# Optimization experiments

Measured on AMD Instinct MI355X. Metric: run time of the kernel, lower is better.

The kernel has to match this reference:

```python
import jax, jax.numpy as jnp
import numpy as np
import math

N_HEAD = 16

def setup_inputs() -> dict:
    key = jax.random.key(0)
    ks = jax.random.split(key, 5)
    B, T, C = 4, 2048, 1024
    x = jax.random.normal(ks[0], (B, T, C), dtype=jnp.float32)
    # xavier-uniform-ish scale for dense kernels
    W_attn = jax.random.normal(ks[1], (C, 3 * C), dtype=jnp.float32) * (1.0 / math.sqrt(C))
    b_attn = jnp.zeros((3 * C,), dtype=jnp.float32)
    W_proj = jax.random.normal(ks[2], (C, C), dtype=jnp.float32) * (1.0 / math.sqrt(C))
    b_proj = jnp.zeros((C,), dtype=jnp.float32)
    return {"x": x, "W_attn": W_attn, "b_attn": b_attn, "W_proj": W_proj, "b_proj": b_proj}

def reference(x, W_attn, b_attn, W_proj, b_proj):
    B, T, C = x.shape
    H = N_HEAD
    D = C // H
    qkv = x @ W_attn + b_attn                      # [B,T,3C]
    q, k, v = jnp.split(qkv, 3, axis=-1)
    q = q.reshape(B, T, H, D).transpose(0, 2, 1, 3)  # [B,H,T,D]
    k = k.reshape(B, T, H, D).transpose(0, 2, 1, 3)
    v = v.reshape(B, T, H, D).transpose(0, 2, 1, 3)
    att = jnp.einsum("bhqd,bhkd->bhqk", q, k) * (1.0 / math.sqrt(D))  # [B,H,T,T]
    causal = jnp.tril(jnp.ones((T, T), dtype=bool))
    att = jnp.where(causal, att, jnp.float32(-jnp.inf))
    att = jax.nn.softmax(att, axis=-1)             # exp(att - logsumexp)
    # dropout rates are 0.0 -> identity
    y = jnp.einsum("bhqk,bhkd->bhqd", att, v)      # [B,H,T,D]
    y = y.transpose(0, 2, 1, 3).reshape(B, T, C)
    y = y @ W_proj + b_proj
    return y
```

## Files before the change

kernel.cpp:

```cpp
#include <hip/hip_runtime.h>
#include <hip/hip_bf16.h>

typedef short s16x8 __attribute__((ext_vector_type(8)));
typedef float f32x4 __attribute__((ext_vector_type(4)));

#define MFMA_BF16(A, B, C) __builtin_amdgcn_mfma_f32_16x16x32_bf16(A, B, C, 0, 0, 0)

constexpr int Bn = 4, Tn = 2048, Cn = 1024, Hn = 16, Dn = 64;
constexpr int Mn = Bn * Tn;
constexpr int Nqkv = 3 * Cn;
constexpr float SC = 0.125f * 1.44269504089f;

__device__ __forceinline__ ushort f2bfu(float f) {
    __hip_bfloat16 h = __float2bfloat16(f);
    return *reinterpret_cast<ushort*>(&h);
}
__device__ __forceinline__ uint pkbf(float a, float b) {
    __hip_bfloat162 h = __float22bfloat162_rn(make_float2(a, b));
    return *reinterpret_cast<uint*>(&h);
}

__device__ __forceinline__ void gl_lds16(const void* g, void* l) {
    __builtin_amdgcn_global_load_lds(
        (const __attribute__((address_space(1))) void*)(uintptr_t)g,
        (__attribute__((address_space(3))) void*)(uint32_t)(uintptr_t)l,
        16, 0, 0);
}

__global__ __launch_bounds__(256) void conv_bf16_kernel(
    const float* __restrict__ src, ushort* __restrict__ dst, int n4)
{
    int i = blockIdx.x * blockDim.x + threadIdx.x;
    int stride = gridDim.x * blockDim.x;
    for (; i < n4; i += stride) {
        float4 v = ((const float4*)src)[i];
        ushort4 o;
        o.x = f2bfu(v.x); o.y = f2bfu(v.y); o.z = f2bfu(v.z); o.w = f2bfu(v.w);
        ((ushort4*)dst)[i] = o;
    }
}

__global__ __launch_bounds__(256) void transpose_cvt_kernel(
    const float* __restrict__ W, ushort* __restrict__ Wt, int K, int N)
{
    __shared__ __align__(16) float Ls[64][68];
    const int t = threadIdx.x;
    const int n0 = blockIdx.x * 64, k0 = blockIdx.y * 64;
#pragma unroll
    for (int p = 0; p < 4; ++p) {
        int r = (t >> 4) + p * 16;
        int c = (t & 15) * 4;
        *(float4*)&Ls[r][c] = *(const float4*)&W[(size_t)(k0 + r) * N + n0 + c];
    }
    __syncthreads();
    const int n = t >> 2;
    const int ks = (t & 3) * 16;
    union { ushort s[16]; uint4 u[2]; } tmp;
#pragma unroll
    for (int j = 0; j < 16; ++j) tmp.s[j] = f2bfu(Ls[ks + j][n]);
    uint4* dp = (uint4*)&Wt[(size_t)(n0 + n) * K + k0 + ks];
    dp[0] = tmp.u[0];
    dp[1] = tmp.u[1];
}

__global__ __launch_bounds__(256) void vt_transpose_kernel(
    const ushort* __restrict__ V, ushort* __restrict__ Vt)
{
    const int tid = threadIdx.x;
    const int bh = blockIdx.x;
    const int kt0 = blockIdx.y * 64;
    const ushort* src = V + (size_t)bh * Tn * Dn;
    ushort* dst = Vt + (size_t)bh * Dn * Tn;
    const int vk = (tid & 15) * 4, vd = (tid >> 4) * 4;
    const ushort* g = src + (size_t)(kt0 + vk) * Dn + vd;
    ushort4 v0 = *(const ushort4*)(g);
    ushort4 v1 = *(const ushort4*)(g + Dn);
    ushort4 v2 = *(const ushort4*)(g + 2 * Dn);
    ushort4 v3 = *(const ushort4*)(g + 3 * Dn);
    ushort4 t0, t1, t2, t3;
    t0.x = v0.x; t0.y = v1.x; t0.z = v2.x; t0.w = v3.x;
    t1.x = v0.y; t1.y = v1.y; t1.z = v2.y; t1.w = v3.y;
    t2.x = v0.z; t2.y = v1.z; t2.z = v2.z; t2.w = v3.z;
    t3.x = v0.w; t3.y = v1.w; t3.z = v2.w; t3.w = v3.w;
    *(ushort4*)(dst + (size_t)(vd + 0) * Tn + kt0 + vk) = t0;
    *(ushort4*)(dst + (size_t)(vd + 1) * Tn + kt0 + vk) = t1;
    *(ushort4*)(dst + (size_t)(vd + 2) * Tn + kt0 + vk) = t2;
    *(ushort4*)(dst + (size_t)(vd + 3) * Tn + kt0 + vk) = t3;
}

__global__ __launch_bounds__(256) void qkv_gemm_mfma(
    const ushort* __restrict__ A, const ushort* __restrict__ Bt,
    const float* __restrict__ bias,
    ushort* __restrict__ Qo, ushort* __restrict__ Ko, ushort* __restrict__ Vo)
{
    __shared__ __align__(16) ushort As[128 * 64];
    __shared__ __align__(16) ushort Bs[128 * 64];
    const int tid = threadIdx.x;
    const int m0 = blockIdx.x * 128, n0 = blockIdx.y * 128;
    const int w = tid >> 6, lane = tid & 63, l15 = lane & 15, qd = lane >> 4;
    const int wm = (w >> 1) * 64, wn = (w & 1) * 64;
    const int lrow = lane >> 3;
    const int lchunk = (lane & 7) ^ (lrow & 7);

    const ushort* gA = A + (size_t)(m0 + w * 32 + lrow) * Cn + lchunk * 8;
    const ushort* gB = Bt + (size_t)(n0 + w * 32 + lrow) * Cn + lchunk * 8;
    ushort* lA = &As[(w * 32) * 64];
    ushort* lB = &Bs[(w * 32) * 64];

    f32x4 acc[4][4] = {};

    for (int k0 = 0; k0 < Cn; k0 += 64) {
        __syncthreads();
#pragma unroll
        for (int t = 0; t < 4; ++t) {
            gl_lds16(gA + (size_t)t * 8 * Cn + k0, lA + t * 8 * 64);
            gl_lds16(gB + (size_t)t * 8 * Cn + k0, lB + t * 8 * 64);
        }
        __syncthreads();
#pragma unroll
        for (int ks = 0; ks < 2; ++ks) {
            const int xs = (((ks * 4 + qd) ^ (l15 & 7))) * 8;
            s16x8 af[4], bfr[4];
#pragma unroll
            for (int i = 0; i < 4; ++i) {
                af[i]  = *(const s16x8*)&As[(wm + i * 16 + l15) * 64 + xs];
                bfr[i] = *(const s16x8*)&Bs[(wn + i * 16 + l15) * 64 + xs];
            }
#pragma unroll
            for (int mt = 0; mt < 4; ++mt)
#pragma unroll
                for (int nt = 0; nt < 4; ++nt)
                    acc[mt][nt] = MFMA_BF16(af[mt], bfr[nt], acc[mt][nt]);
        }
    }

#pragma unroll
    for (int nt = 0; nt < 4; ++nt) {
        int n_g = n0 + wn + nt * 16 + l15;
        float bv = bias[n_g];
        int sel = n_g >> 10;
        int h = (n_g >> 6) & 15;
        int d = n_g & 63;
        ushort* O = (sel == 0) ? Qo : ((sel == 1) ? Ko : Vo);
        float scl = (sel == 0) ? SC : 1.0f;
#pragma unroll
        for (int mt = 0; mt < 4; ++mt) {
#pragma unroll
            for (int r = 0; r < 4; ++r) {
                int m_g = m0 + wm + mt * 16 + qd * 4 + r;
                int b = m_g >> 11, t = m_g & 2047;
                O[(((size_t)(b * Hn + h) * Tn + t) << 6) + d] =
                    f2bfu((acc[mt][nt][r] + bv) * scl);
            }
        }
    }
}

__global__ __launch_bounds__(256, 4) void attn_mfma(
    const ushort* __restrict__ Q, const ushort* __restrict__ K,
    const ushort* __restrict__ Vt, ushort* __restrict__ Y)
{
    __shared__ __align__(16) ushort Ks[2][64 * 64];
    __shared__ __align__(16) ushort Vs[2][64 * 64];
    __shared__ __align__(16) ushort Ps[64 * 64];

    const int tid = threadIdx.x;
    const int bh = blockIdx.x, bx = blockIdx.y;
    const int w = tid >> 6, lane = tid & 63, l15 = lane & 15, qd = lane >> 4;
    const size_t base = (size_t)bh * Tn * Dn;
    const int lrow = lane >> 3;
    const int lchunk = (lane & 7) ^ (lrow & 7);
    const int q_l = w * 16 + l15;
    const int frow = (w * 16 + l15) * 64;
    const int fx0 = ((0 * 4 + qd) ^ (l15 & 7)) * 8;
    const int fx1 = ((1 * 4 + qd) ^ (l15 & 7)) * 8;
    const int b = bh >> 4, h = bh & 15;

    const ushort* Kg = K + base + (size_t)(w * 16 + lrow) * Dn + lchunk * 8;
    const ushort* Vg = Vt + base + (size_t)(w * 16 + lrow) * Tn + lchunk * 8;
    const ushort* Qp = Q + base + (size_t)l15 * Dn + qd * 8;

#pragma unroll
    for (int half = 0; half < 2; ++half) {
        const int qt = half ? (31 - bx) : bx;

        const ushort* qrow = Qp + (size_t)(qt * 64 + w * 16) * Dn;
        s16x8 qf0 = *(const s16x8*)(qrow);
        s16x8 qf1 = *(const s16x8*)(qrow + 32);

        __syncthreads();
#pragma unroll
        for (int t = 0; t < 2; ++t) {
            gl_lds16(Kg + (size_t)(t * 8) * Dn, &Ks[0][(w * 16 + t * 8) * 64]);
            gl_lds16(Vg + (size_t)(t * 8) * Tn, &Vs[0][(w * 16 + t * 8) * 64]);
        }

        float m_run = -1e30f, l_run = 0.f;
        f32x4 o[4] = {};

        for (int kt = 0; kt <= qt; ++kt) {
            const int buf = kt & 1;
            __syncthreads();
            if (kt < qt) {
#pragma unroll
                for (int t = 0; t < 2; ++t) {
                    gl_lds16(Kg + (size_t)((kt + 1) * 64 + t * 8) * Dn,
                             &Ks[buf ^ 1][(w * 16 + t * 8) * 64]);
                    gl_lds16(Vg + (size_t)(t * 8) * Tn + (kt + 1) * 64,
                             &Vs[buf ^ 1][(w * 16 + t * 8) * 64]);
                }
            }

            f32x4 s[4] = {};
#pragma unroll
            for (int nt = 0; nt < 4; ++nt) {
                s16x8 kf = *(const s16x8*)&Ks[buf][(nt * 16 + l15) * 64 + fx0];
                s[nt] = MFMA_BF16(kf, qf0, s[nt]);
            }
#pragma unroll
            for (int nt = 0; nt < 4; ++nt) {
                s16x8 kf = *(const s16x8*)&Ks[buf][(nt * 16 + l15) * 64 + fx1];
                s[nt] = MFMA_BF16(kf, qf1, s[nt]);
            }

            if (kt == qt) {
#pragma unroll
                for (int nt = 0; nt < 4; ++nt)
#pragma unroll
                    for (int r = 0; r < 4; ++r)
                        if (nt * 16 + qd * 4 + r > q_l) s[nt][r] = -1e30f;
            }

            float mx = s[0][0];
#pragma unroll
            for (int nt = 0; nt < 4; ++nt)
#pragma unroll
                for (int r = 0; r < 4; ++r) mx = fmaxf(mx, s[nt][r]);
            mx = fmaxf(mx, __shfl_xor(mx, 16));
            mx = fmaxf(mx, __shfl_xor(mx, 32));

            if (__any(mx > m_run)) {
                float m_new = fmaxf(m_run, mx);
                float alpha = exp2f(m_run - m_new);
                m_run = m_new;
                l_run *= alpha;
#pragma unroll
                for (int dt = 0; dt < 4; ++dt)
#pragma unroll
                    for (int r = 0; r < 4; ++r) o[dt][r] *= alpha;
            }
            float ls = 0.f;
#pragma unroll
            for (int nt = 0; nt < 4; ++nt)
#pragma unroll
                for (int r = 0; r < 4; ++r) {
                    float p = exp2f(s[nt][r] - m_run);
                    s[nt][r] = p;
                    ls += p;
                }
            ls += __shfl_xor(ls, 16);
            ls += __shfl_xor(ls, 32);
            l_run += ls;

#pragma unroll
            for (int nt = 0; nt < 4; ++nt) {
                uint2 pk;
                pk.x = pkbf(s[nt][0], s[nt][1]);
                pk.y = pkbf(s[nt][2], s[nt][3]);
                const int pc = 2 * nt + (qd >> 1), po = (qd & 1) * 4;
                *(uint2*)&Ps[frow + ((pc ^ (l15 & 7)) * 8) + po] = pk;
            }

            {
                s16x8 pb = *(const s16x8*)&Ps[frow + fx0];
#pragma unroll
                for (int dt = 0; dt < 4; ++dt) {
                    s16x8 vf = *(const s16x8*)&Vs[buf][(dt * 16 + l15) * 64 + fx0];
                    o[dt] = MFMA_BF16(vf, pb, o[dt]);
                }
                pb = *(const s16x8*)&Ps[frow + fx1];
#pragma unroll
                for (int dt = 0; dt < 4; ++dt) {
                    s16x8 vf = *(const s16x8*)&Vs[buf][(dt * 16 + l15) * 64 + fx1];
                    o[dt] = MFMA_BF16(vf, pb, o[dt]);
                }
            }
        }

        const float inv = 1.f / l_run;
        const int t_g = qt * 64 + w * 16 + l15;
        ushort* yp = Y + ((size_t)(b * Tn + t_g)) * Cn + h * Dn + qd * 4;
#pragma unroll
        for (int dt = 0; dt < 4; ++dt) {
            uint2 pk;
            pk.x = pkbf(o[dt][0] * inv, o[dt][1] * inv);
            pk.y = pkbf(o[dt][2] * inv, o[dt][3] * inv);
            *(uint2*)(yp + dt * 16) = pk;
        }
    }
}

__global__ __launch_bounds__(256) void proj_gemm_mfma(
    const ushort* __restrict__ A, const ushort* __restrict__ Bt,
    const float* __restrict__ bias, float* __restrict__ out)
{
    __shared__ __align__(16) ushort As[128 * 64];
    __shared__ __align__(16) ushort Bs[128 * 64];
    const int tid = threadIdx.x;
    const int m0 = blockIdx.x * 128, n0 = blockIdx.y * 128;
    const int w = tid >> 6, lane = tid & 63, l15 = lane & 15, qd = lane >> 4;
    const int wm = (w >> 1) * 64, wn = (w & 1) * 64;
    const int lrow = lane >> 3;
    const int lchunk = (lane & 7) ^ (lrow & 7);

    const ushort* gA = A + (size_t)(m0 + w * 32 + lrow) * Cn + lchunk * 8;
    const ushort* gB = Bt + (size_t)(n0 + w * 32 + lrow) * Cn + lchunk * 8;
    ushort* lA = &As[(w * 32) * 64];
    ushort* lB = &Bs[(w * 32) * 64];

    f32x4 acc[4][4] = {};

    for (int k0 = 0; k0 < Cn; k0 += 64) {
        __syncthreads();
#pragma unroll
        for (int t = 0; t < 4; ++t) {
            gl_lds16(gA + (size_t)t * 8 * Cn + k0, lA + t * 8 * 64);
            gl_lds16(gB + (size_t)t * 8 * Cn + k0, lB + t * 8 * 64);
        }
        __syncthreads();
#pragma unroll
        for (int ks = 0; ks < 2; ++ks) {
            const int xs = (((ks * 4 + qd) ^ (l15 & 7))) * 8;
            s16x8 af[4], bfr[4];
#pragma unroll
            for (int i = 0; i < 4; ++i) {
                af[i]  = *(const s16x8*)&As[(wm + i * 16 + l15) * 64 + xs];
                bfr[i] = *(const s16x8*)&Bs[(wn + i * 16 + l15) * 64 + xs];
            }
#pragma unroll
            for (int mt = 0; mt < 4; ++mt)
#pragma unroll
                for (int nt = 0; nt < 4; ++nt)
                    acc[mt][nt] = MFMA_BF16(af[mt], bfr[nt], acc[mt][nt]);
        }
    }

#pragma unroll
    for (int nt = 0; nt < 4; ++nt) {
        int n_g = n0 + wn + nt * 16 + l15;
        float bv = bias[n_g];
#pragma unroll
        for (int mt = 0; mt < 4; ++mt) {
#pragma unroll
            for (int r = 0; r < 4; ++r) {
                int m_g = m0 + wm + mt * 16 + qd * 4 + r;
                out[(size_t)m_g * Cn + n_g] = acc[mt][nt][r] + bv;
            }
        }
    }
}

extern "C" void kernel_launch(void* const* d_in, const int* in_sizes, int n_in,
                              void* d_out, int out_size, void* d_ws, size_t ws_size,
                              hipStream_t stream) {
    const float* x      = (const float*)d_in[0];
    const float* W_attn = (const float*)d_in[1];
    const float* b_attn = (const float*)d_in[2];
    const float* W_proj = (const float*)d_in[3];
    const float* b_proj = (const float*)d_in[4];
    float* out = (float*)d_out;

    constexpr size_t PER = (size_t)Mn * Cn;
    ushort* Qb = (ushort*)d_ws;
    ushort* Kb = Qb + PER;
    ushort* Vb = Kb + PER;
    ushort* Yb = Vb + PER;

    ushort* WtA  = (ushort*)d_out;
    ushort* x_bf = WtA + (size_t)Nqkv * Cn;
    ushort* Vtb  = (ushort*)d_out;
    ushort* WtP  = Qb;

    conv_bf16_kernel<<<1024, 256, 0, stream>>>(x, x_bf, (int)(PER / 4));
    transpose_cvt_kernel<<<dim3(Nqkv / 64, Cn / 64), 256, 0, stream>>>(
        W_attn, WtA, Cn, Nqkv);
    qkv_gemm_mfma<<<dim3(Mn / 128, Nqkv / 128), 256, 0, stream>>>(
        x_bf, WtA, b_attn, Qb, Kb, Vb);
    vt_transpose_kernel<<<dim3(Bn * Hn, Tn / 64), 256, 0, stream>>>(Vb, Vtb);
    attn_mfma<<<dim3(Bn * Hn, 16), 256, 0, stream>>>(Qb, Kb, Vtb, Yb);
    transpose_cvt_kernel<<<dim3(Cn / 64, Cn / 64), 256, 0, stream>>>(
        W_proj, WtP, Cn, Cn);
    proj_gemm_mfma<<<dim3(Mn / 128, Cn / 128), 256, 0, stream>>>(
        Yb, WtP, b_proj, out);
}
```

Before: 267.4 us.

## Use lazy max rescaling, packed FP32 ops, and deferred row-sum reduction in attention

```diff
diff --git a/kernel.cpp b/kernel.cpp
--- a/kernel.cpp
+++ b/kernel.cpp
@@ -3,6 +3,7 @@
 
 typedef short s16x8 __attribute__((ext_vector_type(8)));
 typedef float f32x4 __attribute__((ext_vector_type(4)));
+typedef float f32x2 __attribute__((ext_vector_type(2)));
 
 #define MFMA_BF16(A, B, C) __builtin_amdgcn_mfma_f32_16x16x32_bf16(A, B, C, 0, 0, 0)
 
@@ -18,6 +19,13 @@
 __device__ __forceinline__ uint pkbf(float a, float b) {
     __hip_bfloat162 h = __float22bfloat162_rn(make_float2(a, b));
     return *reinterpret_cast<uint*>(&h);
+}
+
+__device__ __forceinline__ f32x2 pk_add(f32x2 a, f32x2 b) {
+    f32x2 d; asm("v_pk_add_f32 %0, %1, %2" : "=v"(d) : "v"(a), "v"(b)); return d;
+}
+__device__ __forceinline__ f32x2 pk_mul(f32x2 a, f32x2 b) {
+    f32x2 d; asm("v_pk_mul_f32 %0, %1, %2" : "=v"(d) : "v"(a), "v"(b)); return d;
 }
 
 __device__ __forceinline__ void gl_lds16(const void* g, void* l) {
@@ -231,36 +239,42 @@
                         if (nt * 16 + qd * 4 + r > q_l) s[nt][r] = -1e30f;
             }
 
-            float mx = s[0][0];
-#pragma unroll
-            for (int nt = 0; nt < 4; ++nt)
-#pragma unroll
-                for (int r = 0; r < 4; ++r) mx = fmaxf(mx, s[nt][r]);
+            float a0 = fmaxf(fmaxf(s[0][0], s[0][1]), fmaxf(s[0][2], s[0][3]));
+            float a1 = fmaxf(fmaxf(s[1][0], s[1][1]), fmaxf(s[1][2], s[1][3]));
+            float a2 = fmaxf(fmaxf(s[2][0], s[2][1]), fmaxf(s[2][2], s[2][3]));
+            float a3 = fmaxf(fmaxf(s[3][0], s[3][1]), fmaxf(s[3][2], s[3][3]));
+            float mx = fmaxf(fmaxf(a0, a1), fmaxf(a2, a3));
             mx = fmaxf(mx, __shfl_xor(mx, 16));
             mx = fmaxf(mx, __shfl_xor(mx, 32));
 
-            if (__any(mx > m_run)) {
+            if (!__all(mx <= m_run + 8.f)) {
                 float m_new = fmaxf(m_run, mx);
                 float alpha = exp2f(m_run - m_new);
                 m_run = m_new;
                 l_run *= alpha;
-#pragma unroll
-                for (int dt = 0; dt < 4; ++dt)
-#pragma unroll
-                    for (int r = 0; r < 4; ++r) o[dt][r] *= alpha;
-            }
-            float ls = 0.f;
-#pragma unroll
-            for (int nt = 0; nt < 4; ++nt)
-#pragma unroll
-                for (int r = 0; r < 4; ++r) {
-                    float p = exp2f(s[nt][r] - m_run);
-                    s[nt][r] = p;
-                    ls += p;
+                f32x2 aa = {alpha, alpha};
+#pragma unroll
+                for (int dt = 0; dt < 4; ++dt) {
+                    o[dt].lo = pk_mul(o[dt].lo, aa);
+                    o[dt].hi = pk_mul(o[dt].hi, aa);
                 }
-            ls += __shfl_xor(ls, 16);
-            ls += __shfl_xor(ls, 32);
-            l_run += ls;
+            }
+
+            const f32x2 negm = {-m_run, -m_run};
+            f32x2 lac0 = {0.f, 0.f}, lac1 = {0.f, 0.f};
+#pragma unroll
+            for (int nt = 0; nt < 4; ++nt) {
+                s[nt].lo = pk_add(s[nt].lo, negm);
+                s[nt].hi = pk_add(s[nt].hi, negm);
+                s[nt][0] = exp2f(s[nt][0]);
+                s[nt][1] = exp2f(s[nt][1]);
+                s[nt][2] = exp2f(s[nt][2]);
+                s[nt][3] = exp2f(s[nt][3]);
+                lac0 = pk_add(lac0, s[nt].lo);
+                lac1 = pk_add(lac1, s[nt].hi);
+            }
+            lac0 = pk_add(lac0, lac1);
+            l_run += lac0[0] + lac0[1];
 
 #pragma unroll
             for (int nt = 0; nt < 4; ++nt) {
@@ -287,7 +301,10 @@
             }
         }
 
-        const float inv = 1.f / l_run;
+        float lt = l_run;
+        lt += __shfl_xor(lt, 16);
+        lt += __shfl_xor(lt, 32);
+        const float inv = 1.f / lt;
         const int t_g = qt * 64 + w * 16 + l15;
         ushort* yp = Y + ((size_t)(b * Tn + t_g)) * Cn + h * Dn + qd * 4;
 #pragma unroll
```

After: 264.4 us. No clear change (-1.1%).
